# Kernel optimization log

Measured on AMD Instinct MI355X. Metric: run time of the kernel, lower is better.

## Reference

```python
import jax, jax.numpy as jnp
import numpy as np

N = 131072; B = 4; PER = N // B
M = 32768; MPER = M // B; K = 16; E = M * K
NF = 16; C = 32
BNC = float(1.0 / np.sqrt(1.0 + 1e-5))  # BatchNorm1d in eval mode, default running stats (mean=0,var=1,affine=identity)
_kd = np.array([[1.,1.,1.],[-1.,1.,1.],[1.,-1.,1.],[1.,1.,-1.],[-1.,-1.,1.],[-1.,1.,-1.],[1.,-1.,-1.],[-1.,-1.,-1.]], np.float32) / np.float32(np.sqrt(3.0))
KDIRS = jnp.asarray(_kd)  # [8,3] LightKernel directions


def _ln(x, g, b):
    m = x.mean(-1, keepdims=True)
    v = ((x - m) ** 2).mean(-1, keepdims=True)
    return (x - m) / jnp.sqrt(v + 1e-5) * g + b


def _mlp2(x, w1, b1, w2, b2):
    # Seq(Lin, BN, SiLU) x2 ; BN in eval mode == multiply by BNC
    h = jax.nn.silu(BNC * (x @ w1 + b1))
    return jax.nn.silu(BNC * (h @ w2 + b2))


def setup_inputs():
    rng = np.random.default_rng(0)
    f32 = np.float32
    w = lambda fi, fo: jnp.asarray((rng.standard_normal((fi, fo)) * 0.05).astype(f32))
    dg = lambda n: jnp.asarray((rng.standard_normal(n) * 0.05).astype(f32))
    z = lambda n: jnp.zeros((n,), jnp.float32)
    o = lambda n: jnp.ones((n,), jnp.float32)
    pos = jnp.asarray((rng.standard_normal((N, 3)) * 5.0).astype(f32))
    reflectance = jnp.asarray(rng.random(N).astype(f32))
    batch = jnp.asarray(np.repeat(np.arange(B), PER).astype(np.int64))
    sf = jnp.full((B,), 10.0, jnp.float32)
    # voxel-sampled centers: MPER per cloud, within each cloud's index range
    idx = np.concatenate([b * PER + rng.choice(PER, MPER, replace=False) for b in range(B)])
    tb = np.repeat(np.arange(B), MPER)
    # radius-graph edges: K in-batch source neighbors per sampled target
    col = (rng.integers(0, PER, size=(M, K)) + tb[:, None] * PER).reshape(-1)
    row = np.repeat(np.arange(M), K)
    inp = dict(pos=pos, reflectance=reflectance, sf=sf,
               batch=batch, idx=jnp.asarray(idx.astype(np.int64)),
               col=jnp.asarray(col.astype(np.int64)), row=jnp.asarray(row.astype(np.int64)))
    inp.update(stem_ln_g=o(97), stem_ln_b=z(97), stem_w1=w(97, 64), stem_b1=z(64),
               stem_w2=w(64, C), stem_b2=z(C),
               lk_w=w(8, 3), lk_b=z(3), lk_ln_g=o(3), lk_ln_b=z(3),
               loc_w1=w(C + 7, 64), loc_b1=z(64), loc_w2=w(64, 4 * C), loc_b2=z(4 * C),
               exp_w=w(128, 512), exp_b=z(512),
               dw1_w=dg(512), dw1_b=z(512), pw1_w=w(512, 512), pw1_b=z(512),
               dw2_w=dg(512), dw2_b=z(512), pw2_w=w(512, 512), pw2_b=z(512),
               proj_w=w(512, 128), proj_b=z(128))
    return inp


def _forward(pos, reflectance, sf, batch, idx, col, row,
             stem_ln_g, stem_ln_b, stem_w1, stem_b1, stem_w2, stem_b2,
             lk_w, lk_b, lk_ln_g, lk_ln_b,
             loc_w1, loc_b1, loc_w2, loc_b2,
             exp_w, exp_b, dw1_w, dw1_b, pw1_w, pw1_b,
             dw2_w, dw2_b, pw2_w, pw2_b, proj_w, proj_b):
    # --- StemModule: positional encoding + LayerNorm(97) + MLP[97,64,32] ---
    npos = pos / sf[batch][:, None]
    cnt = jax.ops.segment_sum(jnp.ones((N,), jnp.float32), batch, num_segments=B)
    centers = jax.ops.segment_sum(npos, batch, num_segments=B) / jnp.maximum(cnt, 1.0)[:, None]
    npos = npos - centers[batch]
    freqs = 1.0 / (10000.0 ** (2.0 * jnp.arange(NF, dtype=jnp.float32) / NF))
    pe = npos[:, :, None] * freqs                                   # [N,3,NF]
    pe = jnp.concatenate([jnp.sin(pe), jnp.cos(pe)], axis=-1).reshape(N, -1)  # [N,96]
    xin = _ln(jnp.concatenate([pe, reflectance[:, None]], axis=1), stem_ln_g, stem_ln_b)
    x = _mlp2(xin, stem_w1, stem_b1, stem_w2, stem_b2)              # [N,C]
    # --- SAModule: PointNetConv on precomputed radius graph ---
    pos4 = jnp.concatenate([pos, reflectance[:, None]], axis=1)     # [N,4]
    rel = pos4[col] - pos4[idx][row]                                # [E,4] pos_j - pos_i
    rel3 = rel[:, :3]
    dirs = rel3 / (jnp.linalg.norm(rel3, axis=1, keepdims=True) + 1e-8)
    kr = dirs @ KDIRS.T                                             # [E,8] kernel responses
    ecnt = jax.ops.segment_sum(jnp.ones((E,), jnp.float32), row, num_segments=M)
    nb = jax.ops.segment_sum(kr, row, num_segments=M) / jnp.maximum(ecnt, 1.0)[:, None]  # scatter_mean
    sfeat = _ln(nb @ lk_w + lk_b, lk_ln_g, lk_ln_b)                 # [M,3]
    msg = jnp.concatenate([x[col], rel, sfeat[row]], axis=1)        # [E,C+7]
    h = _mlp2(msg, loc_w1, loc_b1, loc_w2, loc_b2)                  # [E,4C] local_nn
    agg = jax.ops.segment_max(h, row, num_segments=M)               # max aggregation [M,4C]
    # --- InvertedResidualBlock (all kernel-size-1 convs => linear / per-channel) ---
    r = agg
    o = jax.nn.silu(BNC * (agg @ exp_w + exp_b))        # expand 128->512
    o = jax.nn.silu(BNC * (o * dw1_w + dw1_b))          # depthwise conv k=1
    o = jax.nn.silu(BNC * (o @ pw1_w + pw1_b))          # pointwise conv
    o = jax.nn.silu(BNC * o)                            # BN+SiLU between DWSep blocks
    o = jax.nn.silu(BNC * (o * dw2_w + dw2_b))
    o = jax.nn.silu(BNC * (o @ pw2_w + pw2_b))
    o = BNC * o                                         # trailing BN (no act)
    o = BNC * (o @ proj_w + proj_b)                     # project 512->128 + BN
    return jax.nn.silu(o + r)                           # [M,4C]


def reference(pos, reflectance, sf, batch, idx, col, row,
              stem_ln_g, stem_ln_b, stem_w1, stem_b1, stem_w2, stem_b2,
              lk_w, lk_b, lk_ln_g, lk_ln_b,
              loc_w1, loc_b1, loc_w2, loc_b2,
              exp_w, exp_b, dw1_w, dw1_b, pw1_w, pw1_b,
              dw2_w, dw2_b, pw2_w, pw2_b, proj_w, proj_b):
    return _forward(pos, reflectance, sf, batch, idx, col, row,
                    stem_ln_g, stem_ln_b, stem_w1, stem_b1, stem_w2, stem_b2,
                    lk_w, lk_b, lk_ln_g, lk_ln_b,
                    loc_w1, loc_b1, loc_w2, loc_b2,
                    exp_w, exp_b, dw1_w, dw1_b, pw1_w, pw1_b,
                    dw2_w, dw2_b, pw2_w, pw2_b, proj_w, proj_b)
```

## Files before the change

kernel.cpp:

```cpp
#include <hip/hip_runtime.h>

typedef unsigned short u16;
typedef unsigned int   u32;
typedef __attribute__((ext_vector_type(8))) u16  u16x8;
typedef __attribute__((ext_vector_type(4))) float f32x4;

#define N_PTS   131072
#define M_PTS   32768
#define BNCF    0.9999950000374997f

__device__ __forceinline__ float b2f(u16 u) {
    u32 x = ((u32)u) << 16;
    float f;
    __builtin_memcpy(&f, &x, 4);
    return f;
}
__device__ __forceinline__ u16 f2b(float f) {
    u32 x;
    __builtin_memcpy(&x, &f, 4);
    u32 r = x + 0x7fffu + ((x >> 16) & 1u);
    return (u16)(r >> 16);
}
__device__ __forceinline__ u16 f2b_hw(float f) {
    u32 r;
    asm("v_cvt_pk_bf16_f32 %0, %1, %1" : "=v"(r) : "v"(f));
    return (u16)r;
}
__device__ __forceinline__ float silu_f(float x) {
    return x * __builtin_amdgcn_rcpf(1.0f + __expf(-x));
}

__device__ __forceinline__ f32x4 mfma_bf16(u16x8 a, u16x8 b, f32x4 c) {
    asm volatile("v_mfma_f32_16x16x32_bf16 %0, %1, %2, %0"
                 : "+v"(c) : "v"(a), "v"(b));
    return c;
}
__device__ __forceinline__ f32x4 acc_fence(f32x4 c) {
    asm volatile("s_nop 7\n\ts_nop 7\n\ts_nop 3" : "+v"(c));
    return c;
}

__device__ __forceinline__ void cp_glds16(const u16* g, u16* l) {
    typedef const __attribute__((address_space(1))) u32* gp1_t;
    typedef __attribute__((address_space(3))) u32* lp3_t;
    __builtin_amdgcn_global_load_lds((gp1_t)(unsigned long long)g,
                                     (lp3_t)(unsigned long long)l, 16, 0, 0);
}

__global__ __launch_bounds__(256) void k_prep(const float* __restrict__ expw, u16* __restrict__ expwt,
                                              const float* __restrict__ pw1w, u16* __restrict__ pw1t,
                                              const float* __restrict__ pw2w, u16* __restrict__ pw2t,
                                              const float* __restrict__ prjw, u16* __restrict__ prjt,
                                              const float* __restrict__ lw1,  u16* __restrict__ lw1t,
                                              const float* __restrict__ lw2,  u16* __restrict__ lw2t,
                                              const float* __restrict__ sw1,  u16* __restrict__ sw1t,
                                              const float* __restrict__ sw2,  u16* __restrict__ sw2t) {
    int idx = blockIdx.x * 256 + threadIdx.x;
    const float* W; u16* O; int K, Kp, Nn;
    if (idx < 65536)                 { W = expw; O = expwt; K = 128; Kp = 128; Nn = 512; }
    else if ((idx -= 65536) < 262144){ W = pw1w; O = pw1t;  K = 512; Kp = 512; Nn = 512; }
    else if ((idx -= 262144) < 262144){ W = pw2w; O = pw2t; K = 512; Kp = 512; Nn = 512; }
    else if ((idx -= 262144) < 65536){ W = prjw; O = prjt;  K = 512; Kp = 512; Nn = 128; }
    else if ((idx -= 65536) < 4096)  { W = lw1;  O = lw1t;  K = 39;  Kp = 64;  Nn = 64;  }
    else if ((idx -= 4096) < 8192)   { W = lw2;  O = lw2t;  K = 64;  Kp = 64;  Nn = 128; }
    else if ((idx -= 8192) < 8192)   { W = sw1;  O = sw1t;  K = 97;  Kp = 128; Nn = 64;  }
    else if ((idx -= 8192) < 2048)   { W = sw2;  O = sw2t;  K = 64;  Kp = 64;  Nn = 32;  }
    else return;
    int n = idx / Kp, k = idx % Kp;
    O[idx] = (k < K) ? f2b(W[(long)k * Nn + n]) : (u16)0;
}

__global__ __launch_bounds__(256) void k_centers(const float* __restrict__ pos,
                                                 const float* __restrict__ sfv,
                                                 const int* __restrict__ batch,
                                                 float* __restrict__ acc) {
    __shared__ float ls[16];
    int t = threadIdx.x;
    if (t < 16) ls[t] = 0.0f;
    __syncthreads();
    int i = blockIdx.x * 256 + t;
    if (i < N_PTS) {
        int b = batch[i];
        float inv = 1.0f / sfv[b];
        atomicAdd(&ls[b * 4 + 0], pos[i * 3 + 0] * inv);
        atomicAdd(&ls[b * 4 + 1], pos[i * 3 + 1] * inv);
        atomicAdd(&ls[b * 4 + 2], pos[i * 3 + 2] * inv);
        atomicAdd(&ls[b * 4 + 3], 1.0f);
    }
    __syncthreads();
    if (t < 16) atomicAdd(&acc[t], ls[t]);
}

__global__ __launch_bounds__(256) void k_stem(const float* __restrict__ pos,
                                              const float* __restrict__ refl,
                                              const float* __restrict__ sfv,
                                              const int* __restrict__ batch,
                                              const float* __restrict__ cacc,
                                              const float* __restrict__ g,
                                              const float* __restrict__ bb,
                                              const u16* __restrict__ w1t,
                                              const float* __restrict__ b1,
                                              const u16* __restrict__ w2t,
                                              const float* __restrict__ b2,
                                              u16* __restrict__ xout) {
    __shared__ u16 xs[128][136];
    __shared__ u16 hb[128][72];
    const float FLO[8] = {
        1.0f, 0.31622776601683794f, 0.1f, 0.031622776601683791f,
        0.01f, 0.0031622776601683794f, 0.001f, 0.00031622776601683794f};
    const float FHI[8] = {
        0.0001f, 3.1622776601683795e-05f, 1e-05f, 3.1622776601683796e-06f,
        1e-06f, 3.1622776601683797e-07f, 1e-07f, 3.1622776601683792e-08f};
    int t = threadIdx.x;
    int wave = t >> 6, lane = t & 63;
    int quad = lane >> 4, l16 = lane & 15;
    int mt0 = wave * 2;

    {
        int p = t >> 1, half = t & 1;
        int i = blockIdx.x * 128 + p;
        int b = batch[i];
        float s = 1.0f / sfv[b];
        float cnt = fmaxf(cacc[b * 4 + 3], 1.0f);
        float npv[3];
#pragma unroll
        for (int d = 0; d < 3; ++d)
            npv[d] = pos[i * 3 + d] * s - cacc[b * 4 + d] / cnt;

        float fq[8];
#pragma unroll
        for (int f = 0; f < 8; ++f) fq[f] = half ? FHI[f] : FLO[f];

        float sv[3][8], cv[3][8];
        float sum = 0.0f, sq = 0.0f;
#pragma unroll
        for (int d = 0; d < 3; ++d) {
#pragma unroll
            for (int f = 0; f < 8; ++f) {
                float a = npv[d] * fq[f];
                float s_, c_;
                __sincosf(a, &s_, &c_);
                sv[d][f] = s_;
                cv[d][f] = c_;
                sum += s_ + c_;
                sq += s_ * s_ + c_ * c_;
            }
        }
        float rf = refl[i];
        if (half == 0) { sum += rf; sq += rf * rf; }
        sum += __shfl_xor(sum, 1);
        sq  += __shfl_xor(sq, 1);

        float m = sum * (1.0f / 97.0f);
        float var = sq * (1.0f / 97.0f) - m * m;
        float rstd = rsqrtf(fmaxf(var, 0.0f) + 1e-5f);

#pragma unroll
        for (int d = 0; d < 3; ++d) {
            int c0 = d * 32 + half * 8;
            {
                f32x4 g0  = *(const f32x4*)(g + c0);
                f32x4 g1  = *(const f32x4*)(g + c0 + 4);
                f32x4 bb0 = *(const f32x4*)(bb + c0);
                f32x4 bb1 = *(const f32x4*)(bb + c0 + 4);
                u16 tmp[8];
#pragma unroll
                for (int f = 0; f < 4; ++f) {
                    float v0 = b2f(f2b(sv[d][f]));
                    tmp[f] = f2b_hw((v0 - m) * rstd * g0[f] + bb0[f]);
                    float v1 = b2f(f2b(sv[d][4 + f]));
                    tmp[4 + f] = f2b_hw((v1 - m) * rstd * g1[f] + bb1[f]);
                }
                *(uint4*)(&xs[p][c0]) = *(uint4*)tmp;
            }
            int c1 = d * 32 + 16 + half * 8;
            {
                f32x4 g0  = *(const f32x4*)(g + c1);
                f32x4 g1  = *(const f32x4*)(g + c1 + 4);
                f32x4 bb0 = *(const f32x4*)(bb + c1);
                f32x4 bb1 = *(const f32x4*)(bb + c1 + 4);
                u16 tmp[8];
#pragma unroll
                for (int f = 0; f < 4; ++f) {
                    float v0 = b2f(f2b(cv[d][f]));
                    tmp[f] = f2b_hw((v0 - m) * rstd * g0[f] + bb0[f]);
                    float v1 = b2f(f2b(cv[d][4 + f]));
                    tmp[4 + f] = f2b_hw((v1 - m) * rstd * g1[f] + bb1[f]);
                }
                *(uint4*)(&xs[p][c1]) = *(uint4*)tmp;
            }
        }
        if (half == 0) {
            float v = b2f(f2b(rf));
            u16 tmp[8];
            tmp[0] = f2b_hw((v - m) * rstd * g[96] + bb[96]);
#pragma unroll
            for (int f = 1; f < 8; ++f) tmp[f] = 0;
            *(uint4*)(&xs[p][96]) = *(uint4*)tmp;
        } else {
            uint4 z = {0, 0, 0, 0};
            *(uint4*)(&xs[p][104]) = z;
            *(uint4*)(&xs[p][112]) = z;
            *(uint4*)(&xs[p][120]) = z;
        }
    }
    __syncthreads();

    {
        f32x4 acc[2][4];
#pragma unroll
        for (int i = 0; i < 2; ++i)
#pragma unroll
            for (int j = 0; j < 4; ++j) acc[i][j] = (f32x4){0.f, 0.f, 0.f, 0.f};
#pragma unroll
        for (int kk = 0; kk < 128; kk += 32) {
            u16x8 af[2], bfr[4];
#pragma unroll
            for (int i = 0; i < 2; ++i)
                af[i] = *(const u16x8*)(&xs[(mt0 + i) * 16 + l16][kk + quad * 8]);
#pragma unroll
            for (int j = 0; j < 4; ++j)
                bfr[j] = *(const u16x8*)(w1t + (j * 16 + l16) * 128 + kk + quad * 8);
#pragma unroll
            for (int i = 0; i < 2; ++i)
#pragma unroll
                for (int j = 0; j < 4; ++j)
                    acc[i][j] = mfma_bf16(af[i], bfr[j], acc[i][j]);
        }
#pragma unroll
        for (int i = 0; i < 2; ++i)
#pragma unroll
            for (int j = 0; j < 4; ++j) {
                f32x4 c = acc_fence(acc[i][j]);
                int n = j * 16 + l16;
                float bn = b1[n] * BNCF;
#pragma unroll
                for (int r = 0; r < 4; ++r)
                    hb[(mt0 + i) * 16 + quad * 4 + r][n] =
                        f2b_hw(silu_f(fmaf(BNCF, c[r], bn)));
            }
    }
    __syncthreads();

    {
        f32x4 acc[2][2];
#pragma unroll
        for (int i = 0; i < 2; ++i)
#pragma unroll
            for (int j = 0; j < 2; ++j) acc[i][j] = (f32x4){0.f, 0.f, 0.f, 0.f};
#pragma unroll
        for (int kk = 0; kk < 64; kk += 32) {
            u16x8 af[2], bfr[2];
#pragma unroll
            for (int i = 0; i < 2; ++i)
                af[i] = *(const u16x8*)(&hb[(mt0 + i) * 16 + l16][kk + quad * 8]);
#pragma unroll
            for (int j = 0; j < 2; ++j)
                bfr[j] = *(const u16x8*)(w2t + (j * 16 + l16) * 64 + kk + quad * 8);
#pragma unroll
            for (int i = 0; i < 2; ++i)
#pragma unroll
                for (int j = 0; j < 2; ++j)
                    acc[i][j] = mfma_bf16(af[i], bfr[j], acc[i][j]);
        }
#pragma unroll
        for (int i = 0; i < 2; ++i)
#pragma unroll
            for (int j = 0; j < 2; ++j) {
                f32x4 c = acc_fence(acc[i][j]);
                int n = j * 16 + l16;
                float bn = b2[n] * BNCF;
#pragma unroll
                for (int r = 0; r < 4; ++r) {
                    int m = (mt0 + i) * 16 + quad * 4 + r;
                    long ig = (long)blockIdx.x * 128 + m;
                    xout[ig * 32 + n] = f2b_hw(silu_f(fmaf(BNCF, c[r], bn)));
                }
            }
    }
}

__global__ __launch_bounds__(256) void k_sfeat(const float* __restrict__ pos,
                                               const int* __restrict__ idxp,
                                               const int* __restrict__ colp,
                                               const float* __restrict__ lkw,
                                               const float* __restrict__ lkb,
                                               const float* __restrict__ lng,
                                               const float* __restrict__ lnb,
                                               float* __restrict__ sfeat) {
    int r = blockIdx.x * 256 + threadIdx.x;
    if (r >= M_PTS) return;
    int ci = idxp[r];
    float cx = pos[ci * 3 + 0];
    float cy = pos[ci * 3 + 1];
    float cz = pos[ci * 3 + 2];
    float dsx = 0.0f, dsy = 0.0f, dsz = 0.0f;
    for (int e = 0; e < 16; ++e) {
        int c = colp[r * 16 + e];
        float dx = pos[c * 3 + 0] - cx;
        float dy = pos[c * 3 + 1] - cy;
        float dz = pos[c * 3 + 2] - cz;
        float nrm = sqrtf(dx * dx + dy * dy + dz * dz);
        float inv = __builtin_amdgcn_rcpf(nrm + 1e-8f);
        dsx += dx * inv;
        dsy += dy * inv;
        dsz += dz * inv;
    }
    const float S3 = 0.57735026918962576f;
    const float sx[8] = {1, -1, 1, 1, -1, -1, 1, -1};
    const float sy[8] = {1, 1, -1, 1, -1, 1, -1, -1};
    const float sz[8] = {1, 1, 1, -1, 1, -1, -1, -1};
    float sc[3] = {lkb[0], lkb[1], lkb[2]};
#pragma unroll
    for (int j = 0; j < 8; ++j) {
        float nb = (sx[j] * dsx + sy[j] * dsy + sz[j] * dsz) * (S3 * (1.0f / 16.0f));
        sc[0] += nb * lkw[j * 3 + 0];
        sc[1] += nb * lkw[j * 3 + 1];
        sc[2] += nb * lkw[j * 3 + 2];
    }
    float m = (sc[0] + sc[1] + sc[2]) * (1.0f / 3.0f);
    float v = ((sc[0] - m) * (sc[0] - m) + (sc[1] - m) * (sc[1] - m) +
               (sc[2] - m) * (sc[2] - m)) * (1.0f / 3.0f);
    float rstd = rsqrtf(fmaxf(v, 0.0f) + 1e-5f);
#pragma unroll
    for (int c = 0; c < 3; ++c)
        sfeat[r * 3 + c] = (sc[c] - m) * rstd * lng[c] + lnb[c];
}

__global__ __launch_bounds__(256) void k_edge(const float* __restrict__ pos,
                                              const float* __restrict__ refl,
                                              const int* __restrict__ idxp,
                                              const int* __restrict__ colp,
                                              const u16* __restrict__ xfeat,
                                              const float* __restrict__ sfeat,
                                              const u16* __restrict__ w1t,
                                              const float* __restrict__ b1,
                                              const u16* __restrict__ w2t,
                                              const float* __restrict__ b2,
                                              float* __restrict__ agg,
                                              u16* __restrict__ aggb) {
    __shared__ u16 uni16[128 * 72];
    __shared__ u16 ws[128 * 72];
    __shared__ float b1s[64];
    __shared__ float b2s[128];
    int t = threadIdx.x;
    int r0 = blockIdx.x * 8;
    long e0 = (long)r0 * 16;
    int wave = t >> 6, lane = t & 63;
    int quad = lane >> 4, l16 = lane & 15;
    int mt0 = wave * 2;

    for (int u = t; u < 512; u += 256) {
        int row = u >> 3, c8 = (u & 7) * 8;
        *(uint4*)(&ws[row * 72 + c8]) = *(const uint4*)(w1t + row * 64 + c8);
    }
    if (t < 64) b1s[t] = b1[t] * BNCF;
    if (t < 128) b2s[t] = b2[t] * BNCF;

    for (int u = t; u < 512; u += 256) {
        int e = u >> 2, seg = u & 3;
        int c = colp[e0 + e];
        uint4 d = *(const uint4*)(xfeat + (long)c * 32 + seg * 8);
        *(uint4*)(&uni16[e * 72 + seg * 8]) = d;
    }
    if (t < 128) {
        int e = t;
        int r = r0 + (e >> 4);
        int c = colp[e0 + e];
        int ci = idxp[r];
        u16 tmp[8];
        tmp[0] = f2b(pos[c * 3 + 0] - pos[ci * 3 + 0]);
        tmp[1] = f2b(pos[c * 3 + 1] - pos[ci * 3 + 1]);
        tmp[2] = f2b(pos[c * 3 + 2] - pos[ci * 3 + 2]);
        tmp[3] = f2b(refl[c] - refl[ci]);
        tmp[4] = f2b(sfeat[r * 3 + 0]);
        tmp[5] = f2b(sfeat[r * 3 + 1]);
        tmp[6] = f2b(sfeat[r * 3 + 2]);
        tmp[7] = 0;
        *(uint4*)(&uni16[e * 72 + 32]) = *(uint4*)tmp;
        uint4 z = {0, 0, 0, 0};
        *(uint4*)(&uni16[e * 72 + 40]) = z;
        *(uint4*)(&uni16[e * 72 + 48]) = z;
        *(uint4*)(&uni16[e * 72 + 56]) = z;
    }
    __syncthreads();

    {
        f32x4 acc[2][4];
#pragma unroll
        for (int i = 0; i < 2; ++i)
#pragma unroll
            for (int j = 0; j < 4; ++j) acc[i][j] = (f32x4){0.f, 0.f, 0.f, 0.f};
#pragma unroll
        for (int kk = 0; kk < 64; kk += 32) {
            u16x8 af[2], bfr[4];
#pragma unroll
            for (int i = 0; i < 2; ++i)
                af[i] = *(const u16x8*)(&uni16[((mt0 + i) * 16 + l16) * 72 + kk + quad * 8]);
#pragma unroll
            for (int j = 0; j < 4; ++j)
                bfr[j] = *(const u16x8*)(&ws[(j * 16 + l16) * 72 + kk + quad * 8]);
#pragma unroll
            for (int i = 0; i < 2; ++i)
#pragma unroll
                for (int j = 0; j < 4; ++j)
                    acc[i][j] = mfma_bf16(af[i], bfr[j], acc[i][j]);
        }
#pragma unroll
        for (int i = 0; i < 2; ++i)
#pragma unroll
            for (int j = 0; j < 4; ++j) {
                f32x4 c = acc_fence(acc[i][j]);
                int n = j * 16 + l16;
#pragma unroll
                for (int r = 0; r < 4; ++r) {
                    float v = silu_f(fmaf(BNCF, c[r], b1s[n]));
                    uni16[((mt0 + i) * 16 + quad * 4 + r) * 72 + n] = f2b_hw(v);
                }
            }
    }
    __syncthreads();

    for (int u = t; u < 1024; u += 256) {
        int row = u >> 3, c8 = (u & 7) * 8;
        *(uint4*)(&ws[row * 72 + c8]) = *(const uint4*)(w2t + row * 64 + c8);
    }
    __syncthreads();

    {
        f32x4 acc[2][8];
#pragma unroll
        for (int i = 0; i < 2; ++i)
#pragma unroll
            for (int j = 0; j < 8; ++j) acc[i][j] = (f32x4){0.f, 0.f, 0.f, 0.f};
#pragma unroll
        for (int kk = 0; kk < 64; kk += 32) {
            u16x8 af[2], bfr[8];
#pragma unroll
            for (int i = 0; i < 2; ++i)
                af[i] = *(const u16x8*)(&uni16[((mt0 + i) * 16 + l16) * 72 + kk + quad * 8]);
#pragma unroll
            for (int j = 0; j < 8; ++j)
                bfr[j] = *(const u16x8*)(&ws[(j * 16 + l16) * 72 + kk + quad * 8]);
#pragma unroll
            for (int i = 0; i < 2; ++i)
#pragma unroll
                for (int j = 0; j < 8; ++j)
                    acc[i][j] = mfma_bf16(af[i], bfr[j], acc[i][j]);
        }
#pragma unroll
        for (int i = 0; i < 2; ++i) {
            int rg = r0 + mt0 + i;
#pragma unroll
            for (int j = 0; j < 8; ++j) {
                f32x4 c = acc_fence(acc[i][j]);
                int n = j * 16 + l16;
                float mx = fmaxf(fmaxf(c[0], c[1]), fmaxf(c[2], c[3]));
                float mn = fminf(fminf(c[0], c[1]), fminf(c[2], c[3]));
                mx = fmaxf(mx, __shfl_xor(mx, 16));
                mx = fmaxf(mx, __shfl_xor(mx, 32));
                mn = fminf(mn, __shfl_xor(mn, 16));
                mn = fminf(mn, __shfl_xor(mn, 32));
                if (quad == 0) {
                    float v = fmaxf(silu_f(fmaf(BNCF, mx, b2s[n])),
                                    silu_f(fmaf(BNCF, mn, b2s[n])));
                    agg[(long)rg * 128 + n] = v;
                    aggb[(long)rg * 128 + n] = f2b_hw(v);
                }
            }
        }
    }
}

template <int EPI, int OD>
__global__ __launch_bounds__(256) void k_mgemm(const u16* __restrict__ A,
                                               const u16* __restrict__ Bt,
                                               const float* __restrict__ bias,
                                               const float* __restrict__ dww,
                                               const float* __restrict__ dwb,
                                               const float* __restrict__ res,
                                               void* __restrict__ Ov,
                                               int K, int Nn) {
    __shared__ u16 As[128 * 64];
    __shared__ u16 Bs[128 * 64];
    int t = threadIdx.x;
    int wave = t >> 6, lane = t & 63;
    int quad = lane >> 4, l16 = lane & 15;
    int R0 = blockIdx.y * 128, C0 = blockIdx.x * 128;
    int wm = (wave & 1) * 64, wn = (wave >> 1) * 64;

    int srow = (lane >> 3);
    int sch  = lane & 7;

    f32x4 acc[4][4];
#pragma unroll
    for (int i = 0; i < 4; ++i)
#pragma unroll
        for (int j = 0; j < 4; ++j) acc[i][j] = (f32x4){0.f, 0.f, 0.f, 0.f};

    for (int k0 = 0; k0 < K; k0 += 64) {
#pragma unroll
        for (int it = 0; it < 4; ++it) {
            int base = wave * 32 + it * 8;
            int row = base + srow;
            int gch = (sch ^ (row & 7)) << 3;
            cp_glds16(A  + (long)(R0 + row) * K + k0 + gch, &As[base * 64]);
            cp_glds16(Bt + (long)(C0 + row) * K + k0 + gch, &Bs[base * 64]);
        }
        __syncthreads();
#pragma unroll
        for (int kk = 0; kk < 64; kk += 32) {
            int kb = kk >> 3;
            u16x8 af[4], bfr[4];
#pragma unroll
            for (int tm = 0; tm < 4; ++tm) {
                int r = wm + tm * 16 + l16;
                af[tm] = *(const u16x8*)(&As[r * 64 + (((kb + quad) ^ (r & 7)) << 3)]);
            }
#pragma unroll
            for (int tn = 0; tn < 4; ++tn) {
                int r = wn + tn * 16 + l16;
                bfr[tn] = *(const u16x8*)(&Bs[r * 64 + (((kb + quad) ^ (r & 7)) << 3)]);
            }
#pragma unroll
            for (int tm = 0; tm < 4; ++tm)
#pragma unroll
                for (int tn = 0; tn < 4; ++tn)
                    acc[tm][tn] = mfma_bf16(af[tm], bfr[tn], acc[tm][tn]);
        }
        __syncthreads();
    }

#pragma unroll
    for (int tm = 0; tm < 4; ++tm) {
#pragma unroll
        for (int tn = 0; tn < 4; ++tn) {
            f32x4 c = acc_fence(acc[tm][tn]);
            int n = C0 + wn + tn * 16 + l16;
            float bn = bias[n] * BNCF;
            float dn = 0.0f, db = 0.0f;
            if (EPI == 0 || EPI == 1) { dn = dww[n] * BNCF; db = dwb[n] * BNCF; }
#pragma unroll
            for (int r = 0; r < 4; ++r) {
                int m = R0 + wm + tm * 16 + quad * 4 + r;
                float v = c[r];
                if (EPI == 0) {
                    v = silu_f(fmaf(BNCF, v, bn));
                    v = silu_f(fmaf(v, dn, db));
                } else if (EPI == 1) {
                    v = silu_f(fmaf(BNCF, v, bn));
                    v = silu_f(BNCF * v);
                    v = silu_f(fmaf(v, dn, db));
                } else if (EPI == 2) {
                    v = silu_f(fmaf(BNCF, v, bn));
                    v = BNCF * v;
                } else {
                    v = fmaf(BNCF, v, bn);
                    v = silu_f(v + res[(long)m * 128 + n]);
                }
                if (OD == 0)
                    ((u16*)Ov)[(long)m * Nn + n] = f2b_hw(v);
                else
                    ((float*)Ov)[(long)m * Nn + n] = v;
            }
        }
    }
}

extern "C" void kernel_launch(void* const* d_in, const int* in_sizes, int n_in,
                              void* d_out, int out_size, void* d_ws, size_t ws_size,
                              hipStream_t stream) {
    const float* pos   = (const float*)d_in[0];
    const float* refl  = (const float*)d_in[1];
    const float* sfv   = (const float*)d_in[2];
    const int*   batch = (const int*)d_in[3];
    const int*   idxp  = (const int*)d_in[4];
    const int*   colp  = (const int*)d_in[5];
    const float* s_g  = (const float*)d_in[7];
    const float* s_b  = (const float*)d_in[8];
    const float* s_w1 = (const float*)d_in[9];
    const float* s_b1 = (const float*)d_in[10];
    const float* s_w2 = (const float*)d_in[11];
    const float* s_b2 = (const float*)d_in[12];
    const float* lkw  = (const float*)d_in[13];
    const float* lkb  = (const float*)d_in[14];
    const float* lng  = (const float*)d_in[15];
    const float* lnb  = (const float*)d_in[16];
    const float* l_w1 = (const float*)d_in[17];
    const float* l_b1 = (const float*)d_in[18];
    const float* l_w2 = (const float*)d_in[19];
    const float* l_b2 = (const float*)d_in[20];
    const float* expw = (const float*)d_in[21];
    const float* expb = (const float*)d_in[22];
    const float* dw1w = (const float*)d_in[23];
    const float* dw1b = (const float*)d_in[24];
    const float* pw1w = (const float*)d_in[25];
    const float* pw1b = (const float*)d_in[26];
    const float* dw2w = (const float*)d_in[27];
    const float* dw2b = (const float*)d_in[28];
    const float* pw2w = (const float*)d_in[29];
    const float* pw2b = (const float*)d_in[30];
    const float* prjw = (const float*)d_in[31];
    const float* prjb = (const float*)d_in[32];

    char* ws = (char*)d_ws;
    float* cent  = (float*)(ws + 0);
    float* sfeat = (float*)(ws + 64);
    float* agg   = (float*)(ws + 393280);
    u16*   aggb  = (u16*)(ws + 17170496);
    u16*   u1    = (u16*)(ws + 25559104);
    u16*   u2    = (u16*)(ws + 59113536);
    u16*   xf    = (u16*)(ws + 59113536);
    u16*   expwt = (u16*)(ws + 92667968);
    u16*   pw1t  = (u16*)(ws + 92799040);
    u16*   pw2t  = (u16*)(ws + 93323328);
    u16*   prjt  = (u16*)(ws + 93847616);
    u16*   lw1t  = (u16*)(ws + 93978688);
    u16*   lw2t  = (u16*)(ws + 93986880);
    u16*   sw1t  = (u16*)(ws + 94003264);
    u16*   sw2t  = (u16*)(ws + 94019648);

    k_prep<<<2648, 256, 0, stream>>>(expw, expwt, pw1w, pw1t, pw2w, pw2t,
                                     prjw, prjt, l_w1, lw1t, l_w2, lw2t,
                                     s_w1, sw1t, s_w2, sw2t);

    hipMemsetAsync(cent, 0, 64, stream);
    k_centers<<<512, 256, 0, stream>>>(pos, sfv, batch, cent);
    k_stem<<<1024, 256, 0, stream>>>(pos, refl, sfv, batch, cent, s_g, s_b,
                                     sw1t, s_b1, sw2t, s_b2, xf);
    k_sfeat<<<128, 256, 0, stream>>>(pos, idxp, colp, lkw, lkb, lng, lnb, sfeat);
    k_edge<<<4096, 256, 0, stream>>>(pos, refl, idxp, colp, xf, sfeat,
                                     lw1t, l_b1, lw2t, l_b2, agg, aggb);

    dim3 blk(256);
    k_mgemm<0, 0><<<dim3(4, 256), blk, 0, stream>>>(aggb, expwt, expb, dw1w, dw1b,
                                                    nullptr, u1, 128, 512);
    k_mgemm<1, 0><<<dim3(4, 256), blk, 0, stream>>>(u1, pw1t, pw1b, dw2w, dw2b,
                                                    nullptr, u2, 512, 512);
    k_mgemm<2, 0><<<dim3(4, 256), blk, 0, stream>>>(u2, pw2t, pw2b, nullptr, nullptr,
                                                    nullptr, u1, 512, 512);
    k_mgemm<3, 1><<<dim3(1, 256), blk, 0, stream>>>(u1, prjt, prjb, nullptr, nullptr,
                                                    agg, d_out, 512, 128);
}
```

Baseline: 333.1 us.

## Fuse surface-feature kernel into edge kernel and tweak launch bounds and conversions

Removes the separate k_sfeat kernel and computes the LightKernel surface features inside k_edge, using a 16-lane xor-shuffle reduction over each target's edges. This drops one launch and the sfeat round trip through memory. It also drops the redundant double bf16 rounding in the stem LayerNorm, switches edge conversions to the hardware bf16 convert, replaces div/mod with shifts in the weight prep, and adds min-blocks launch-bound hints to k_stem, k_edge and k_mgemm. The occupancy hints may force register spills, and skipping the pre-rounding changes numerics slightly.

```diff
diff --git a/kernel.cpp b/kernel.cpp
--- a/kernel.cpp
+++ b/kernel.cpp
@@ -56,17 +56,17 @@
                                               const float* __restrict__ sw1,  u16* __restrict__ sw1t,
                                               const float* __restrict__ sw2,  u16* __restrict__ sw2t) {
     int idx = blockIdx.x * 256 + threadIdx.x;
-    const float* W; u16* O; int K, Kp, Nn;
-    if (idx < 65536)                 { W = expw; O = expwt; K = 128; Kp = 128; Nn = 512; }
-    else if ((idx -= 65536) < 262144){ W = pw1w; O = pw1t;  K = 512; Kp = 512; Nn = 512; }
-    else if ((idx -= 262144) < 262144){ W = pw2w; O = pw2t; K = 512; Kp = 512; Nn = 512; }
-    else if ((idx -= 262144) < 65536){ W = prjw; O = prjt;  K = 512; Kp = 512; Nn = 128; }
-    else if ((idx -= 65536) < 4096)  { W = lw1;  O = lw1t;  K = 39;  Kp = 64;  Nn = 64;  }
-    else if ((idx -= 4096) < 8192)   { W = lw2;  O = lw2t;  K = 64;  Kp = 64;  Nn = 128; }
-    else if ((idx -= 8192) < 8192)   { W = sw1;  O = sw1t;  K = 97;  Kp = 128; Nn = 64;  }
-    else if ((idx -= 8192) < 2048)   { W = sw2;  O = sw2t;  K = 64;  Kp = 64;  Nn = 32;  }
+    const float* W; u16* O; int K, ksh, Nn;
+    if (idx < 65536)                 { W = expw; O = expwt; K = 128; ksh = 7; Nn = 512; }
+    else if ((idx -= 65536) < 262144){ W = pw1w; O = pw1t;  K = 512; ksh = 9; Nn = 512; }
+    else if ((idx -= 262144) < 262144){ W = pw2w; O = pw2t; K = 512; ksh = 9; Nn = 512; }
+    else if ((idx -= 262144) < 65536){ W = prjw; O = prjt;  K = 512; ksh = 9; Nn = 128; }
+    else if ((idx -= 65536) < 4096)  { W = lw1;  O = lw1t;  K = 39;  ksh = 6; Nn = 64;  }
+    else if ((idx -= 4096) < 8192)   { W = lw2;  O = lw2t;  K = 64;  ksh = 6; Nn = 128; }
+    else if ((idx -= 8192) < 8192)   { W = sw1;  O = sw1t;  K = 97;  ksh = 7; Nn = 64;  }
+    else if ((idx -= 8192) < 2048)   { W = sw2;  O = sw2t;  K = 64;  ksh = 6; Nn = 32;  }
     else return;
-    int n = idx / Kp, k = idx % Kp;
+    int n = idx >> ksh, k = idx & ((1 << ksh) - 1);
     O[idx] = (k < K) ? f2b(W[(long)k * Nn + n]) : (u16)0;
 }
 
@@ -91,7 +91,7 @@
     if (t < 16) atomicAdd(&acc[t], ls[t]);
 }
 
-__global__ __launch_bounds__(256) void k_stem(const float* __restrict__ pos,
+__global__ __launch_bounds__(256, 3) void k_stem(const float* __restrict__ pos,
                                               const float* __restrict__ refl,
                                               const float* __restrict__ sfv,
                                               const int* __restrict__ batch,
@@ -166,10 +166,8 @@
                 u16 tmp[8];
 #pragma unroll
                 for (int f = 0; f < 4; ++f) {
-                    float v0 = b2f(f2b(sv[d][f]));
-                    tmp[f] = f2b_hw((v0 - m) * rstd * g0[f] + bb0[f]);
-                    float v1 = b2f(f2b(sv[d][4 + f]));
-                    tmp[4 + f] = f2b_hw((v1 - m) * rstd * g1[f] + bb1[f]);
+                    tmp[f]     = f2b_hw((sv[d][f]     - m) * rstd * g0[f] + bb0[f]);
+                    tmp[4 + f] = f2b_hw((sv[d][4 + f] - m) * rstd * g1[f] + bb1[f]);
                 }
                 *(uint4*)(&xs[p][c0]) = *(uint4*)tmp;
             }
@@ -182,16 +180,14 @@
                 u16 tmp[8];
 #pragma unroll
                 for (int f = 0; f < 4; ++f) {
-                    float v0 = b2f(f2b(cv[d][f]));
-                    tmp[f] = f2b_hw((v0 - m) * rstd * g0[f] + bb0[f]);
-                    float v1 = b2f(f2b(cv[d][4 + f]));
-                    tmp[4 + f] = f2b_hw((v1 - m) * rstd * g1[f] + bb1[f]);
+                    tmp[f]     = f2b_hw((cv[d][f]     - m) * rstd * g0[f] + bb0[f]);
+                    tmp[4 + f] = f2b_hw((cv[d][4 + f] - m) * rstd * g1[f] + bb1[f]);
                 }
                 *(uint4*)(&xs[p][c1]) = *(uint4*)tmp;
             }
         }
         if (half == 0) {
-            float v = b2f(f2b(rf));
+            float v = rf;
             u16 tmp[8];
             tmp[0] = f2b_hw((v - m) * rstd * g[96] + bb[96]);
 #pragma unroll
@@ -280,59 +276,15 @@
     }
 }
 
-__global__ __launch_bounds__(256) void k_sfeat(const float* __restrict__ pos,
-                                               const int* __restrict__ idxp,
-                                               const int* __restrict__ colp,
-                                               const float* __restrict__ lkw,
-                                               const float* __restrict__ lkb,
-                                               const float* __restrict__ lng,
-                                               const float* __restrict__ lnb,
-                                               float* __restrict__ sfeat) {
-    int r = blockIdx.x * 256 + threadIdx.x;
-    if (r >= M_PTS) return;
-    int ci = idxp[r];
-    float cx = pos[ci * 3 + 0];
-    float cy = pos[ci * 3 + 1];
-    float cz = pos[ci * 3 + 2];
-    float dsx = 0.0f, dsy = 0.0f, dsz = 0.0f;
-    for (int e = 0; e < 16; ++e) {
-        int c = colp[r * 16 + e];
-        float dx = pos[c * 3 + 0] - cx;
-        float dy = pos[c * 3 + 1] - cy;
-        float dz = pos[c * 3 + 2] - cz;
-        float nrm = sqrtf(dx * dx + dy * dy + dz * dz);
-        float inv = __builtin_amdgcn_rcpf(nrm + 1e-8f);
-        dsx += dx * inv;
-        dsy += dy * inv;
-        dsz += dz * inv;
-    }
-    const float S3 = 0.57735026918962576f;
-    const float sx[8] = {1, -1, 1, 1, -1, -1, 1, -1};
-    const float sy[8] = {1, 1, -1, 1, -1, 1, -1, -1};
-    const float sz[8] = {1, 1, 1, -1, 1, -1, -1, -1};
-    float sc[3] = {lkb[0], lkb[1], lkb[2]};
-#pragma unroll
-    for (int j = 0; j < 8; ++j) {
-        float nb = (sx[j] * dsx + sy[j] * dsy + sz[j] * dsz) * (S3 * (1.0f / 16.0f));
-        sc[0] += nb * lkw[j * 3 + 0];
-        sc[1] += nb * lkw[j * 3 + 1];
-        sc[2] += nb * lkw[j * 3 + 2];
-    }
-    float m = (sc[0] + sc[1] + sc[2]) * (1.0f / 3.0f);
-    float v = ((sc[0] - m) * (sc[0] - m) + (sc[1] - m) * (sc[1] - m) +
-               (sc[2] - m) * (sc[2] - m)) * (1.0f / 3.0f);
-    float rstd = rsqrtf(fmaxf(v, 0.0f) + 1e-5f);
-#pragma unroll
-    for (int c = 0; c < 3; ++c)
-        sfeat[r * 3 + c] = (sc[c] - m) * rstd * lng[c] + lnb[c];
-}
-
-__global__ __launch_bounds__(256) void k_edge(const float* __restrict__ pos,
+__global__ __launch_bounds__(256, 4) void k_edge(const float* __restrict__ pos,
                                               const float* __restrict__ refl,
                                               const int* __restrict__ idxp,
                                               const int* __restrict__ colp,
                                               const u16* __restrict__ xfeat,
-                                              const float* __restrict__ sfeat,
+                                              const float* __restrict__ lkw,
+                                              const float* __restrict__ lkb,
+                                              const float* __restrict__ lng,
+                                              const float* __restrict__ lnb,
                                               const u16* __restrict__ w1t,
                                               const float* __restrict__ b1,
                                               const u16* __restrict__ w2t,
@@ -368,14 +320,45 @@
         int r = r0 + (e >> 4);
         int c = colp[e0 + e];
         int ci = idxp[r];
+        float dx = pos[c * 3 + 0] - pos[ci * 3 + 0];
+        float dy = pos[c * 3 + 1] - pos[ci * 3 + 1];
+        float dz = pos[c * 3 + 2] - pos[ci * 3 + 2];
+        float dr = refl[c] - refl[ci];
+
+        float nrm = sqrtf(dx * dx + dy * dy + dz * dz);
+        float inv = __builtin_amdgcn_rcpf(nrm + 1e-8f);
+        float ux = dx * inv, uy = dy * inv, uz = dz * inv;
+#pragma unroll
+        for (int msk = 1; msk <= 8; msk <<= 1) {
+            ux += __shfl_xor(ux, msk);
+            uy += __shfl_xor(uy, msk);
+            uz += __shfl_xor(uz, msk);
+        }
+        const float S3_16 = 0.57735026918962576f * (1.0f / 16.0f);
+        const float sxk[8] = {1, -1, 1, 1, -1, -1, 1, -1};
+        const float syk[8] = {1, 1, -1, 1, -1, 1, -1, -1};
+        const float szk[8] = {1, 1, 1, -1, 1, -1, -1, -1};
+        float sc0 = lkb[0], sc1 = lkb[1], sc2 = lkb[2];
+#pragma unroll
+        for (int j = 0; j < 8; ++j) {
+            float nb = (sxk[j] * ux + syk[j] * uy + szk[j] * uz) * S3_16;
+            sc0 += nb * lkw[j * 3 + 0];
+            sc1 += nb * lkw[j * 3 + 1];
+            sc2 += nb * lkw[j * 3 + 2];
+        }
+        float mm = (sc0 + sc1 + sc2) * (1.0f / 3.0f);
+        float vv = ((sc0 - mm) * (sc0 - mm) + (sc1 - mm) * (sc1 - mm) +
+                    (sc2 - mm) * (sc2 - mm)) * (1.0f / 3.0f);
+        float rstd = rsqrtf(fmaxf(vv, 0.0f) + 1e-5f);
+
         u16 tmp[8];
-        tmp[0] = f2b(pos[c * 3 + 0] - pos[ci * 3 + 0]);
-        tmp[1] = f2b(pos[c * 3 + 1] - pos[ci * 3 + 1]);
-        tmp[2] = f2b(pos[c * 3 + 2] - pos[ci * 3 + 2]);
-        tmp[3] = f2b(refl[c] - refl[ci]);
-        tmp[4] = f2b(sfeat[r * 3 + 0]);
-        tmp[5] = f2b(sfeat[r * 3 + 1]);
-        tmp[6] = f2b(sfeat[r * 3 + 2]);
+        tmp[0] = f2b_hw(dx);
+        tmp[1] = f2b_hw(dy);
+        tmp[2] = f2b_hw(dz);
+        tmp[3] = f2b_hw(dr);
+        tmp[4] = f2b_hw((sc0 - mm) * rstd * lng[0] + lnb[0]);
+        tmp[5] = f2b_hw((sc1 - mm) * rstd * lng[1] + lnb[1]);
+        tmp[6] = f2b_hw((sc2 - mm) * rstd * lng[2] + lnb[2]);
         tmp[7] = 0;
         *(uint4*)(&uni16[e * 72 + 32]) = *(uint4*)tmp;
         uint4 z = {0, 0, 0, 0};
@@ -473,7 +456,7 @@
 }
 
 template <int EPI, int OD>
-__global__ __launch_bounds__(256) void k_mgemm(const u16* __restrict__ A,
+__global__ __launch_bounds__(256, 4) void k_mgemm(const u16* __restrict__ A,
                                                const u16* __restrict__ Bt,
                                                const float* __restrict__ bias,
                                                const float* __restrict__ dww,
@@ -605,7 +588,6 @@
 
     char* ws = (char*)d_ws;
     float* cent  = (float*)(ws + 0);
-    float* sfeat = (float*)(ws + 64);
     float* agg   = (float*)(ws + 393280);
     u16*   aggb  = (u16*)(ws + 17170496);
     u16*   u1    = (u16*)(ws + 25559104);
@@ -628,8 +610,8 @@
     k_centers<<<512, 256, 0, stream>>>(pos, sfv, batch, cent);
     k_stem<<<1024, 256, 0, stream>>>(pos, refl, sfv, batch, cent, s_g, s_b,
                                      sw1t, s_b1, sw2t, s_b2, xf);
-    k_sfeat<<<128, 256, 0, stream>>>(pos, idxp, colp, lkw, lkb, lng, lnb, sfeat);
-    k_edge<<<4096, 256, 0, stream>>>(pos, refl, idxp, colp, xf, sfeat,
+    k_edge<<<4096, 256, 0, stream>>>(pos, refl, idxp, colp, xf,
+                                     lkw, lkb, lng, lnb,
                                      lw1t, l_b1, lw2t, l_b2, agg, aggb);
 
     dim3 blk(256);
```

Measured after the change: 322.5 us. 3.2% less time.
